# Kernel tuning notes

Hardware: AMD Instinct MI355X
Metric: run time of the kernel (lower is better)

## Reference

```python
import jax, jax.numpy as jnp
import numpy as np

N, E, D = 50000, 800000, 128
RESIDUAL_SCALE = 1.0
EPS = 1e-5  # torch LayerNorm default eps


def _mlp_ln(h, w1, b1, w2, b2, w3, b3, g, beta):
    # MeshGraphNets MLP: Linear -> SiLU -> Linear -> SiLU -> Linear -> LayerNorm
    h = jax.nn.silu(h @ w1 + b1)
    h = jax.nn.silu(h @ w2 + b2)
    h = h @ w3 + b3
    mu = h.mean(axis=-1, keepdims=True)
    var = ((h - mu) ** 2).mean(axis=-1, keepdims=True)
    return g * (h - mu) * jax.lax.rsqrt(var + EPS) + beta


def setup_inputs() -> dict:
    key = jax.random.key(0)
    ks = jax.random.split(key, 16)

    def lin(k, fan_in, fan_out):
        bound = 1.0 / np.sqrt(fan_in)
        kw, kb = jax.random.split(k)
        w = jax.random.uniform(kw, (fan_in, fan_out), jnp.float32, -bound, bound)
        b = jax.random.uniform(kb, (fan_out,), jnp.float32, -bound, bound)
        return w, b

    x = jax.random.normal(ks[0], (N, D), jnp.float32)
    edge_attr = jax.random.normal(ks[1], (E, D), jnp.float32)
    edge_index = jax.random.randint(ks[2], (2, E), 0, N, jnp.int32)

    ew1, eb1 = lin(ks[3], 3 * D, D)
    ew2, eb2 = lin(ks[4], D, D)
    ew3, eb3 = lin(ks[5], D, D)
    e_gamma = jnp.ones((D,), jnp.float32)
    e_beta = jnp.zeros((D,), jnp.float32)

    nw1, nb1 = lin(ks[6], 2 * D, D)
    nw2, nb2 = lin(ks[7], D, D)
    nw3, nb3 = lin(ks[8], D, D)
    n_gamma = jnp.ones((D,), jnp.float32)
    n_beta = jnp.zeros((D,), jnp.float32)

    return dict(x=x, edge_attr=edge_attr, edge_index=edge_index,
                ew1=ew1, eb1=eb1, ew2=ew2, eb2=eb2, ew3=ew3, eb3=eb3,
                e_gamma=e_gamma, e_beta=e_beta,
                nw1=nw1, nb1=nb1, nw2=nw2, nb2=nb2, nw3=nw3, nb3=nb3,
                n_gamma=n_gamma, n_beta=n_beta)


def reference(x, edge_attr, edge_index,
              ew1, eb1, ew2, eb2, ew3, eb3, e_gamma, e_beta,
              nw1, nb1, nw2, nb2, nw3, nb3, n_gamma, n_beta):
    senders, receivers = edge_index[0], edge_index[1]

    # EdgeBlock: gather endpoint node features, concat with edge_attr, MLP
    edge_in = jnp.concatenate([x[senders], x[receivers], edge_attr], axis=-1)  # [E, 3D]
    edge_mlp_out = _mlp_ln(edge_in, ew1, eb1, ew2, eb2, ew3, eb3, e_gamma, e_beta)  # [E, D]

    # NodeBlock: scatter-sum edge messages to receiver nodes, concat with x, MLP
    agg = jax.ops.segment_sum(edge_mlp_out, receivers, num_segments=N)  # [N, D]
    node_in = jnp.concatenate([x, agg], axis=-1)  # [N, 2D]
    node_mlp_out = _mlp_ln(node_in, nw1, nb1, nw2, nb2, nw3, nb3, n_gamma, n_beta)

    # Residual updates
    x_new = x + RESIDUAL_SCALE * node_mlp_out

    # PairNorm (use_pairnorm=True)
    x_centered = x_new - x_new.mean(axis=0, keepdims=True)
    rms = jnp.linalg.norm(x_centered) / jnp.sqrt(jnp.float32(x_new.shape[0])) + 1e-8
    x_new = x_centered / rms

    edge_attr_new = edge_attr + RESIDUAL_SCALE * edge_mlp_out
    return x_new, edge_attr_new
```

## Files before the change

### kernel.cpp

```cpp
#include <hip/hip_runtime.h>
#include <hip/hip_bf16.h>

#define NN 50000
#define NE 800000
#define ROWB 272

typedef unsigned short u16;
typedef unsigned int u32;
typedef __attribute__((ext_vector_type(4))) float f32x4;
typedef __attribute__((ext_vector_type(8))) short short8;


__device__ __forceinline__ u16 f2b(float f){ __hip_bfloat16 h = __float2bfloat16(f); u16 u; __builtin_memcpy(&u, &h, 2); return u; }
__device__ __forceinline__ float b2f(u16 u){ __hip_bfloat16 h; __builtin_memcpy(&h, &u, 2); return __bfloat162float(h); }
__device__ __forceinline__ float siluf(float v){
  const float e = __expf(-v);
  return v * __builtin_amdgcn_rcpf(1.f + e);
}

__device__ __forceinline__ uint4 cvt8(const float* __restrict__ s){
  const float4 a = *(const float4*)s;
  const float4 b = *(const float4*)(s + 4);
  union { u16 h[8]; uint4 q; } u;
  u.h[0]=f2b(a.x); u.h[1]=f2b(a.y); u.h[2]=f2b(a.z); u.h[3]=f2b(a.w);
  u.h[4]=f2b(b.x); u.h[5]=f2b(b.y); u.h[6]=f2b(b.z); u.h[7]=f2b(b.w);
  return u.q;
}

template<int K>
__device__ __forceinline__ void gemm128(f32x4 acc[4][2], const u16* __restrict__ sA,
                                        const u16* __restrict__ wB, int wm, int wn, int lane){
  const int l15 = lane & 15, l4 = lane >> 4;
  const u16* w0 = wB + (size_t)(wn*32 + l15)*K + l4*8;
  const u16* w1 = w0 + (size_t)16*K;
  #pragma unroll
  for (int ks = 0; ks < 4; ++ks){
    const short8 b0 = *(const short8*)(w0 + ks*32);
    const short8 b1 = *(const short8*)(w1 + ks*32);
    const int kb = ks*64 + l4*16;
    short8 a[4];
    #pragma unroll
    for (int fr = 0; fr < 4; ++fr)
      a[fr] = *(const short8*)((const char*)sA + (wm*64 + fr*16 + l15)*ROWB + kb);
    #pragma unroll
    for (int fr = 0; fr < 4; ++fr){
      acc[fr][0] = __builtin_amdgcn_mfma_f32_16x16x32_bf16(a[fr], b0, acc[fr][0], 0, 0, 0);
      acc[fr][1] = __builtin_amdgcn_mfma_f32_16x16x32_bf16(a[fr], b1, acc[fr][1], 0, 0, 0);
    }
  }
}

template<int K>
__device__ __forceinline__ void gemm64(f32x4 acc[2][4], const u16* __restrict__ sA,
                                       const u16* __restrict__ wB, int wm, int wn, int lane){
  const int l15 = lane & 15, l4 = lane >> 4;
  const u16* w0 = wB + (size_t)(wn*64 + l15)*K + l4*8;
  #pragma unroll
  for (int ks = 0; ks < 4; ++ks){
    short8 b[4];
    #pragma unroll
    for (int fc = 0; fc < 4; ++fc)
      b[fc] = *(const short8*)(w0 + (size_t)fc*16*K + ks*32);
    const int kb = ks*64 + l4*16;
    short8 a[2];
    #pragma unroll
    for (int fr = 0; fr < 2; ++fr)
      a[fr] = *(const short8*)((const char*)sA + (wm*32 + fr*16 + l15)*ROWB + kb);
    #pragma unroll
    for (int fr = 0; fr < 2; ++fr)
      #pragma unroll
      for (int fc = 0; fc < 4; ++fc)
        acc[fr][fc] = __builtin_amdgcn_mfma_f32_16x16x32_bf16(a[fr], b[fc], acc[fr][fc], 0, 0, 0);
  }
}

__device__ __forceinline__ void epilogue(const f32x4 acc[4][2], const float* __restrict__ bias,
                                         u16* __restrict__ dst, int wm, int wn, int lane, bool doSilu){
  const int l15 = lane & 15, l4 = lane >> 4;
  #pragma unroll
  for (int fc = 0; fc < 2; ++fc){
    const int col = wn*32 + fc*16 + l15;
    const float bv = bias[col];
    #pragma unroll
    for (int fr = 0; fr < 4; ++fr){
      const int rbase = wm*64 + fr*16 + l4*4;
      #pragma unroll
      for (int j = 0; j < 4; ++j){
        float v = acc[fr][fc][j] + bv;
        if (doSilu) v = siluf(v);
        *(u16*)((char*)dst + (rbase + j)*ROWB + col*2) = f2b(v);
      }
    }
  }
}

__device__ __forceinline__ void epilogue64(const f32x4 acc[2][4], const float* __restrict__ bias,
                                           u16* __restrict__ dst, int wm, int wn, int lane, bool doSilu){
  const int l15 = lane & 15, l4 = lane >> 4;
  #pragma unroll
  for (int fc = 0; fc < 4; ++fc){
    const int col = wn*64 + fc*16 + l15;
    const float bv = bias[col];
    #pragma unroll
    for (int fr = 0; fr < 2; ++fr){
      const int rbase = wm*32 + fr*16 + l4*4;
      #pragma unroll
      for (int j = 0; j < 4; ++j){
        float v = acc[fr][fc][j] + bv;
        if (doSilu) v = siluf(v);
        *(u16*)((char*)dst + (rbase + j)*ROWB + col*2) = f2b(v);
      }
    }
  }
}

__global__ __launch_bounds__(256) void prep_kernel(const float* __restrict__ w1, const float* __restrict__ w2,
                                                   const float* __restrict__ w3, const float* __restrict__ m1,
                                                   const float* __restrict__ m2, const float* __restrict__ m3,
                                                   u16* __restrict__ wt,
                                                   const float* __restrict__ x, u16* __restrict__ xB,
                                                   const int* __restrict__ eidx, int* __restrict__ cnt){
  const int i = blockIdx.x * 256 + threadIdx.x;
  if (i < 147456){
    const float* src; int K, base, off;
    if      (i < 49152)  { src = w1; K = 384; base = 0;      off = i; }
    else if (i < 65536)  { src = w2; K = 128; base = 49152;  off = i - 49152; }
    else if (i < 81920)  { src = w3; K = 128; base = 65536;  off = i - 65536; }
    else if (i < 114688) { src = m1; K = 256; base = 81920;  off = i - 81920; }
    else if (i < 131072) { src = m2; K = 128; base = 114688; off = i - 114688; }
    else                 { src = m3; K = 128; base = 131072; off = i - 131072; }
    const int k = off >> 7, n = off & 127;
    wt[base + n*K + k] = f2b(src[off]);
  }
  if (xB){
    const size_t o = (size_t)i * 8;
    *(uint4*)(xB + o) = cvt8(x + o);
  }
  atomicAdd(&cnt[eidx[NE + i]], 1);
}

__global__ __launch_bounds__(1024) void scan_kernel(const int* __restrict__ cnt, int* __restrict__ off,
                                                    int* __restrict__ cursor){
  __shared__ int s[1024];
  const int t = threadIdx.x;
  const int CH = 49;
  int sum = 0;
  for (int i = 0; i < CH; ++i){
    const int idx = t*CH + i;
    if (idx < NN) sum += cnt[idx];
  }
  s[t] = sum;
  __syncthreads();
  for (int d = 1; d < 1024; d <<= 1){
    int v = (t >= d) ? s[t - d] : 0;
    __syncthreads();
    s[t] += v;
    __syncthreads();
  }
  int run = s[t] - sum;
  for (int i = 0; i < CH; ++i){
    const int idx = t*CH + i;
    if (idx < NN){
      off[idx] = run;
      cursor[idx] = run;
      run += cnt[idx];
      if (idx == NN - 1) off[NN] = run;
    }
  }
}

__global__ __launch_bounds__(256) void scatter_kernel(const int* __restrict__ eidx, int* __restrict__ cursor,
                                                      int* __restrict__ perm, int* __restrict__ slot){
  const int i = blockIdx.x * 256 + threadIdx.x;
  if (i < NE){
    const int pos = atomicAdd(&cursor[eidx[NE + i]], 1);
    perm[pos] = i;
    slot[i] = pos;
  }
}

__global__ __launch_bounds__(256, 4) void pre_kernel(const float* __restrict__ x, const u16* __restrict__ xB,
                                                     const u16* __restrict__ wt, u16* __restrict__ Pab){
  __shared__ u16 sX[64*136];
  const int t = threadIdx.x;
  const int nBase = blockIdx.x * 64;
  const int lane = t & 63, wid = t >> 6;
  const int wm = wid >> 1, wn = wid & 1;
  const int chunk = t & 15, r0 = t >> 4;

  #pragma unroll
  for (int p = 0; p < 4; ++p){
    const int row = r0 + p*16;
    const int node = nBase + row;
    uint4 v = {0u, 0u, 0u, 0u};
    if (node < NN){
      if (xB) v = *(const uint4*)(xB + (size_t)node*128 + chunk*8);
      else    v = cvt8(x + (size_t)node*128 + chunk*8);
    }
    *(uint4*)((char*)sX + row*ROWB + chunk*16) = v;
  }
  __syncthreads();

  const f32x4 z4 = {0.f, 0.f, 0.f, 0.f};
  const int l15 = lane & 15, l4 = lane >> 4;
  #pragma unroll
  for (int half = 0; half < 2; ++half){
    f32x4 acc[2][4];
    #pragma unroll
    for (int fr = 0; fr < 2; ++fr)
      #pragma unroll
      for (int fc = 0; fc < 4; ++fc) acc[fr][fc] = z4;
    gemm64<384>(acc, sX, wt + half*128, wm, wn, lane);
    #pragma unroll
    for (int fc = 0; fc < 4; ++fc){
      const int col = wn*64 + fc*16 + l15;
      #pragma unroll
      for (int fr = 0; fr < 2; ++fr){
        const int rbase = wm*32 + fr*16 + l4*4;
        #pragma unroll
        for (int j = 0; j < 4; ++j){
          const int node = nBase + rbase + j;
          if (node < NN) Pab[(size_t)node*256 + half*128 + col] = f2b(acc[fr][fc][j]);
        }
      }
    }
  }
}

__global__ __launch_bounds__(512, 4) void edge_kernel(
    const float* __restrict__ ea, const int* __restrict__ eidx,
    const u16* __restrict__ wt, const u16* __restrict__ Pab,
    const float* __restrict__ b1, const float* __restrict__ b2,
    const float* __restrict__ b3, const float* __restrict__ gma, const float* __restrict__ bta,
    const int* __restrict__ slot, float* __restrict__ outE, u16* __restrict__ oBuf)
{
  __shared__ u16 sA[128*136];
  __shared__ float sMeta[640];
  __shared__ int sIdx[256];
  __shared__ int sSlot[128];
  const int t = threadIdx.x;
  const size_t eBase = (size_t)blockIdx.x * 128;

  if (t < 128){
    sIdx[t]       = eidx[eBase + t];
    sIdx[t + 128] = eidx[(size_t)NE + eBase + t];
    sSlot[t]      = slot[eBase + t];
    sMeta[t]       = b1[t];
    sMeta[t + 128] = b2[t];
    sMeta[t + 256] = b3[t];
    sMeta[t + 384] = gma[t];
    sMeta[t + 512] = bta[t];
  }
  __syncthreads();

  const int lane = t & 63, wid = t >> 6;
  const int wm = wid >> 2, wn = wid & 3;
  const int chunk = t & 15, r0 = t >> 4;
  const int l15 = lane & 15, l4 = lane >> 4;

  uint4 eaQ[4];
  #pragma unroll
  for (int p = 0; p < 4; ++p){
    const int row = r0 + p*32;
    uint4 v = cvt8(ea + ((eBase + row)*128 + chunk*8));
    eaQ[p] = v;
    *(uint4*)((char*)sA + row*ROWB + chunk*16) = v;
  }

  f32x4 acc[4][2];
  #pragma unroll
  for (int fr = 0; fr < 4; ++fr){
    #pragma unroll
    for (int j = 0; j < 4; ++j){
      const int row = wm*64 + fr*16 + l4*4 + j;
      const u16* pa = Pab + (size_t)sIdx[row]*256;
      const u16* pb = Pab + (size_t)sIdx[row + 128]*256 + 128;
      #pragma unroll
      for (int fc = 0; fc < 2; ++fc){
        const int col = wn*32 + fc*16 + l15;
        acc[fr][fc][j] = b2f(pa[col]) + b2f(pb[col]);
      }
    }
  }
  __syncthreads();

  gemm128<384>(acc, sA, wt + 256, wm, wn, lane);
  __syncthreads();
  epilogue(acc, sMeta + 0, sA, wm, wn, lane, true);
  __syncthreads();
  const f32x4 z4 = {0.f, 0.f, 0.f, 0.f};
  #pragma unroll
  for (int fr = 0; fr < 4; ++fr){ acc[fr][0] = z4; acc[fr][1] = z4; }
  gemm128<128>(acc, sA, wt + 49152, wm, wn, lane);
  __syncthreads();
  epilogue(acc, sMeta + 128, sA, wm, wn, lane, true);
  __syncthreads();
  #pragma unroll
  for (int fr = 0; fr < 4; ++fr){ acc[fr][0] = z4; acc[fr][1] = z4; }
  gemm128<128>(acc, sA, wt + 65536, wm, wn, lane);
  __syncthreads();
  epilogue(acc, sMeta + 256, sA, wm, wn, lane, false);
  __syncthreads();

  {
    #pragma unroll
    for (int p = 0; p < 4; ++p){
      const int row = r0 + p*32;
      uint4 q = *(const uint4*)((const char*)sA + row*ROWB + chunk*16);
      const u16* pu = (const u16*)&q;
      float h[8];
      #pragma unroll
      for (int j = 0; j < 8; ++j) h[j] = b2f(pu[j]);
      float s = 0.f;
      #pragma unroll
      for (int j = 0; j < 8; ++j) s += h[j];
      s += __shfl_xor(s, 1); s += __shfl_xor(s, 2); s += __shfl_xor(s, 4); s += __shfl_xor(s, 8);
      const float mu = s * (1.f/128.f);
      float ss = 0.f;
      #pragma unroll
      for (int j = 0; j < 8; ++j){ const float d = h[j] - mu; ss += d*d; }
      ss += __shfl_xor(ss, 1); ss += __shfl_xor(ss, 2); ss += __shfl_xor(ss, 4); ss += __shfl_xor(ss, 8);
      const float rs = rsqrtf(fmaxf(ss*(1.f/128.f), 0.f) + 1e-5f);
      const size_t e = eBase + row;
      const u16* ep = (const u16*)&eaQ[p];
      alignas(16) float orow[8];
      alignas(16) u16 obf[8];
      #pragma unroll
      for (int j = 0; j < 8; ++j){
        const int col = chunk*8 + j;
        const float o = sMeta[384 + col]*(h[j] - mu)*rs + sMeta[512 + col];
        orow[j] = b2f(ep[j]) + o;
        obf[j] = f2b(o);
      }
      float* dst = outE + e*128 + chunk*8;
      *(float4*)dst       = ((const float4*)orow)[0];
      *(float4*)(dst + 4) = ((const float4*)orow)[1];
      if (oBuf) *(uint4*)(oBuf + (size_t)sSlot[row]*128 + chunk*8) = *(const uint4*)obf;
    }
  }
}

__global__ __launch_bounds__(256) void agg_f_kernel(const float* __restrict__ outE, const float* __restrict__ ea,
                                                    const int* __restrict__ off, const int* __restrict__ perm,
                                                    float* __restrict__ agg){
  const int node = blockIdx.x * 4 + (threadIdx.x >> 6);
  const int lane = threadIdx.x & 63;
  if (node >= NN) return;
  const int s = off[node], e = off[node + 1];
  float a0 = 0.f, a1 = 0.f;
  for (int i = s; i < e; ++i){
    const size_t r = (size_t)perm[i] * 128;
    a0 += outE[r + lane]      - ea[r + lane];
    a1 += outE[r + 64 + lane] - ea[r + 64 + lane];
  }
  agg[(size_t)node*128 + lane]      = a0;
  agg[(size_t)node*128 + 64 + lane] = a1;
}

__global__ __launch_bounds__(256, 4) void node_kernel(
    const float* __restrict__ x, const float* __restrict__ aggF,
    const u16* __restrict__ oBuf, const int* __restrict__ off,
    const u16* __restrict__ wt,
    const float* __restrict__ b1, const float* __restrict__ b2, const float* __restrict__ b3,
    const float* __restrict__ gma, const float* __restrict__ bta,
    float* __restrict__ outX, float* __restrict__ stats)
{
  __shared__ u16 sA[64*136];
  __shared__ float sMeta[640];
  __shared__ float sCol[128];
  __shared__ float sSq;
  const int t = threadIdx.x;
  const int nBase = blockIdx.x * 64;

  if (t < 128){
    sMeta[t]       = b1[t];
    sMeta[t + 128] = b2[t];
    sMeta[t + 256] = b3[t];
    sMeta[t + 384] = gma[t];
    sMeta[t + 512] = bta[t];
    sCol[t] = 0.f;
  }
  if (t == 0) sSq = 0.f;
  __syncthreads();

  const int lane = t & 63, wid = t >> 6;
  const int wm = wid >> 1, wn = wid & 1;
  const int chunk = t & 15, r0 = t >> 4;

  const f32x4 z4 = {0.f, 0.f, 0.f, 0.f};
  f32x4 acc[2][4];
  #pragma unroll
  for (int fr = 0; fr < 2; ++fr)
    #pragma unroll
    for (int fc = 0; fc < 4; ++fc) acc[fr][fc] = z4;

  for (int kc = 0; kc < 2; ++kc){
    #pragma unroll
    for (int p = 0; p < 4; ++p){
      const int row = r0 + p*16;
      const int node = nBase + row;
      uint4 v = {0u, 0u, 0u, 0u};
      if (node < NN){
        if (kc == 0){
          v = cvt8(x + (size_t)node*128 + chunk*8);
        } else if (oBuf){
          float a[8] = {0.f,0.f,0.f,0.f,0.f,0.f,0.f,0.f};
          const int s0 = off[node], e0 = off[node + 1];
          for (int i = s0; i < e0; ++i){
            uint4 q = *(const uint4*)(oBuf + (size_t)i*128 + chunk*8);
            const u16* pu = (const u16*)&q;
            #pragma unroll
            for (int j = 0; j < 8; ++j) a[j] += b2f(pu[j]);
          }
          union { u16 h[8]; uint4 q; } u;
          #pragma unroll
          for (int j = 0; j < 8; ++j) u.h[j] = f2b(a[j]);
          v = u.q;
        } else {
          v = cvt8(aggF + (size_t)node*128 + chunk*8);
        }
      }
      *(uint4*)((char*)sA + row*ROWB + chunk*16) = v;
    }
    __syncthreads();
    gemm64<256>(acc, sA, wt + 81920 + kc*128, wm, wn, lane);
    __syncthreads();
  }
  epilogue64(acc, sMeta + 0, sA, wm, wn, lane, true);
  __syncthreads();
  #pragma unroll
  for (int fr = 0; fr < 2; ++fr)
    #pragma unroll
    for (int fc = 0; fc < 4; ++fc) acc[fr][fc] = z4;
  gemm64<128>(acc, sA, wt + 114688, wm, wn, lane);
  __syncthreads();
  epilogue64(acc, sMeta + 128, sA, wm, wn, lane, true);
  __syncthreads();
  #pragma unroll
  for (int fr = 0; fr < 2; ++fr)
    #pragma unroll
    for (int fc = 0; fc < 4; ++fc) acc[fr][fc] = z4;
  gemm64<128>(acc, sA, wt + 131072, wm, wn, lane);
  __syncthreads();
  epilogue64(acc, sMeta + 256, sA, wm, wn, lane, false);
  __syncthreads();

  {
    float lssq = 0.f;
    #pragma unroll
    for (int p = 0; p < 4; ++p){
      const int row = r0 + p*16;
      const int node = nBase + row;
      uint4 q = *(const uint4*)((const char*)sA + row*ROWB + chunk*16);
      const u16* pu = (const u16*)&q;
      float h[8];
      #pragma unroll
      for (int j = 0; j < 8; ++j) h[j] = b2f(pu[j]);
      float s = 0.f;
      #pragma unroll
      for (int j = 0; j < 8; ++j) s += h[j];
      s += __shfl_xor(s, 1); s += __shfl_xor(s, 2); s += __shfl_xor(s, 4); s += __shfl_xor(s, 8);
      const float mu = s * (1.f/128.f);
      float ss = 0.f;
      #pragma unroll
      for (int j = 0; j < 8; ++j){ const float d = h[j] - mu; ss += d*d; }
      ss += __shfl_xor(ss, 1); ss += __shfl_xor(ss, 2); ss += __shfl_xor(ss, 4); ss += __shfl_xor(ss, 8);
      const float rs = rsqrtf(fmaxf(ss*(1.f/128.f), 0.f) + 1e-5f);
      if (node < NN){
        const float* xRow = x + (size_t)node*128 + chunk*8;
        const float4 xa = *(const float4*)xRow;
        const float4 xb = *(const float4*)(xRow + 4);
        float xr[8] = {xa.x, xa.y, xa.z, xa.w, xb.x, xb.y, xb.z, xb.w};
        alignas(16) float orow[8];
        #pragma unroll
        for (int j = 0; j < 8; ++j){
          const int col = chunk*8 + j;
          const float o = sMeta[384 + col]*(h[j] - mu)*rs + sMeta[512 + col];
          const float res = xr[j] + o;
          orow[j] = res;
          atomicAdd(&sCol[col], res);
          lssq += res*res;
        }
        float* dst = outX + (size_t)node*128 + chunk*8;
        *(float4*)dst       = ((const float4*)orow)[0];
        *(float4*)(dst + 4) = ((const float4*)orow)[1];
      }
    }
    #pragma unroll
    for (int m = 1; m < 64; m <<= 1) lssq += __shfl_xor(lssq, m);
    if (lane == 0) atomicAdd(&sSq, lssq);
  }
  __syncthreads();
  if (t < 128) atomicAdd(&stats[t], sCol[t]);
  if (t == 0)  atomicAdd(&stats[128], sSq);
}

__global__ __launch_bounds__(256) void pairnorm_kernel(float* __restrict__ xOut, const float* __restrict__ stats){
  __shared__ float sMean[128];
  __shared__ float sP2[2];
  __shared__ float sInv;
  const int t = threadIdx.x;
  float m2 = 0.f;
  if (t < 128){
    const float mean = stats[t] * (1.f / (float)NN);
    sMean[t] = mean;
    m2 = mean * mean;
  }
  #pragma unroll
  for (int m = 1; m < 64; m <<= 1) m2 += __shfl_xor(m2, m);
  if ((t & 63) == 0 && t < 128) sP2[t >> 6] = m2;
  __syncthreads();
  if (t == 0){
    float ssc = stats[128] - (float)NN * (sP2[0] + sP2[1]);
    ssc = fmaxf(ssc, 0.f);
    const float rms = sqrtf(ssc * (1.f / (float)NN)) + 1e-8f;
    sInv = 1.f / rms;
  }
  __syncthreads();
  const size_t base = ((size_t)blockIdx.x * 256 + t) * 4;
  const int col = (int)(base & 127);
  float4 q = *(float4*)(xOut + base);
  const float inv = sInv;
  q.x = (q.x - sMean[col])     * inv;
  q.y = (q.y - sMean[col + 1]) * inv;
  q.z = (q.z - sMean[col + 2]) * inv;
  q.w = (q.w - sMean[col + 3]) * inv;
  *(float4*)(xOut + base) = q;
}

extern "C" void kernel_launch(void* const* d_in, const int* in_sizes, int n_in,
                              void* d_out, int out_size, void* d_ws, size_t ws_size,
                              hipStream_t stream){
  (void)in_sizes; (void)n_in; (void)out_size;
  const float* x    = (const float*)d_in[0];
  const float* ea   = (const float*)d_in[1];
  const int*   eidx = (const int*)d_in[2];
  const float* ew1  = (const float*)d_in[3];
  const float* eb1  = (const float*)d_in[4];
  const float* ew2  = (const float*)d_in[5];
  const float* eb2  = (const float*)d_in[6];
  const float* ew3  = (const float*)d_in[7];
  const float* eb3  = (const float*)d_in[8];
  const float* eg   = (const float*)d_in[9];
  const float* ebt  = (const float*)d_in[10];
  const float* nw1  = (const float*)d_in[11];
  const float* nb1  = (const float*)d_in[12];
  const float* nw2  = (const float*)d_in[13];
  const float* nb2  = (const float*)d_in[14];
  const float* nw3  = (const float*)d_in[15];
  const float* nb3  = (const float*)d_in[16];
  const float* ng   = (const float*)d_in[17];
  const float* nbt  = (const float*)d_in[18];

  u16*   wt     = (u16*)d_ws;
  float* stats  = (float*)((char*)d_ws + 294912);
  int*   cnt    = (int*)((char*)d_ws + 297216);
  int*   off    = (int*)((char*)d_ws + 497408);
  int*   cursor = (int*)((char*)d_ws + 697600);
  int*   perm   = (int*)((char*)d_ws + 897792);
  int*   slot   = (int*)((char*)d_ws + 4097792);
  const bool useO = ws_size >= (7297792ull + (size_t)NE * 128 * 2);
  const bool useX = ws_size >= (7297792ull + (size_t)NE * 128 * 2 + (size_t)NN * 128 * 2);
  u16*   oBuf   = useO ? (u16*)((char*)d_ws + 7297792) : (u16*)nullptr;
  u16*   xB     = useX ? (u16*)((char*)d_ws + 7297792 + (size_t)NE * 128 * 2) : (u16*)nullptr;
  float* outX   = (float*)d_out;
  u16*   Pab    = (u16*)d_out;
  float* outE   = outX + (size_t)NN * 128;

  hipMemsetAsync(stats, 0, 2048, stream);
  hipMemsetAsync(cnt, 0, NN * sizeof(int), stream);
  prep_kernel<<<3125, 256, 0, stream>>>(ew1, ew2, ew3, nw1, nw2, nw3, wt, x, xB, eidx, cnt);
  scan_kernel<<<1, 1024, 0, stream>>>(cnt, off, cursor);
  scatter_kernel<<<3125, 256, 0, stream>>>(eidx, cursor, perm, slot);
  pre_kernel<<<782, 256, 0, stream>>>(x, xB, wt, Pab);
  edge_kernel<<<6250, 512, 0, stream>>>(ea, eidx, wt, Pab, eb1, eb2, eb3, eg, ebt, slot, outE, oBuf);
  if (!useO) agg_f_kernel<<<12500, 256, 0, stream>>>(outE, ea, off, perm, outX);
  node_kernel<<<782, 256, 0, stream>>>(x, outX, oBuf, off, wt, nb1, nb2, nb3, ng, nbt, outX, stats);
  pairnorm_kernel<<<6250, 256, 0, stream>>>(outX, stats);
}
```

Baseline: 723.2 us.

## Fuse scan into precompute kernel and assign CSR slots inside edge kernel

Merges the single-block prefix scan into the node precompute kernel as an extra block, and drops the separate scatter pass on the bf16 output path by claiming each edge's CSR slot with an atomic on the cursor inside the edge kernel. The two memsets are combined into one. This removes kernel launches and a full pass over edge indices. In exchange the scan now runs on 256 threads instead of 1024. Slot order within a segment becomes nondeterministic, and the edge kernel's atomics contend on hot receivers.

```diff
diff --git a/kernel.cpp b/kernel.cpp
--- a/kernel.cpp
+++ b/kernel.cpp
@@ -139,51 +139,51 @@
   atomicAdd(&cnt[eidx[NE + i]], 1);
 }
 
-__global__ __launch_bounds__(1024) void scan_kernel(const int* __restrict__ cnt, int* __restrict__ off,
-                                                    int* __restrict__ cursor){
-  __shared__ int s[1024];
-  const int t = threadIdx.x;
-  const int CH = 49;
-  int sum = 0;
-  for (int i = 0; i < CH; ++i){
-    const int idx = t*CH + i;
-    if (idx < NN) sum += cnt[idx];
-  }
-  s[t] = sum;
-  __syncthreads();
-  for (int d = 1; d < 1024; d <<= 1){
-    int v = (t >= d) ? s[t - d] : 0;
-    __syncthreads();
-    s[t] += v;
-    __syncthreads();
-  }
-  int run = s[t] - sum;
-  for (int i = 0; i < CH; ++i){
-    const int idx = t*CH + i;
-    if (idx < NN){
-      off[idx] = run;
-      cursor[idx] = run;
-      run += cnt[idx];
-      if (idx == NN - 1) off[NN] = run;
-    }
-  }
-}
-
 __global__ __launch_bounds__(256) void scatter_kernel(const int* __restrict__ eidx, int* __restrict__ cursor,
-                                                      int* __restrict__ perm, int* __restrict__ slot){
+                                                      int* __restrict__ perm){
   const int i = blockIdx.x * 256 + threadIdx.x;
   if (i < NE){
     const int pos = atomicAdd(&cursor[eidx[NE + i]], 1);
     perm[pos] = i;
-    slot[i] = pos;
-  }
-}
-
-__global__ __launch_bounds__(256, 4) void pre_kernel(const float* __restrict__ x, const u16* __restrict__ xB,
-                                                     const u16* __restrict__ wt, u16* __restrict__ Pab){
+  }
+}
+
+__global__ __launch_bounds__(256, 4) void scanpre_kernel(const int* __restrict__ cnt, int* __restrict__ off,
+                                                         int* __restrict__ cursor,
+                                                         const float* __restrict__ x, const u16* __restrict__ xB,
+                                                         const u16* __restrict__ wt, u16* __restrict__ Pab){
+  const int t = threadIdx.x;
+  if (blockIdx.x == 0){
+    __shared__ int s[256];
+    const int CH = 196;
+    int sum = 0;
+    for (int i = 0; i < CH; ++i){
+      const int idx = t*CH + i;
+      if (idx < NN) sum += cnt[idx];
+    }
+    s[t] = sum;
+    __syncthreads();
+    for (int d = 1; d < 256; d <<= 1){
+      int v = (t >= d) ? s[t - d] : 0;
+      __syncthreads();
+      s[t] += v;
+      __syncthreads();
+    }
+    int run = s[t] - sum;
+    for (int i = 0; i < CH; ++i){
+      const int idx = t*CH + i;
+      if (idx < NN){
+        off[idx] = run;
+        cursor[idx] = run;
+        run += cnt[idx];
+        if (idx == NN - 1) off[NN] = run;
+      }
+    }
+    return;
+  }
+
   __shared__ u16 sX[64*136];
-  const int t = threadIdx.x;
-  const int nBase = blockIdx.x * 64;
+  const int nBase = (blockIdx.x - 1) * 64;
   const int lane = t & 63, wid = t >> 6;
   const int wm = wid >> 1, wn = wid & 1;
   const int chunk = t & 15, r0 = t >> 4;
@@ -232,7 +232,7 @@
     const u16* __restrict__ wt, const u16* __restrict__ Pab,
     const float* __restrict__ b1, const float* __restrict__ b2,
     const float* __restrict__ b3, const float* __restrict__ gma, const float* __restrict__ bta,
-    const int* __restrict__ slot, float* __restrict__ outE, u16* __restrict__ oBuf)
+    int* __restrict__ cursor, float* __restrict__ outE, u16* __restrict__ oBuf)
 {
   __shared__ u16 sA[128*136];
   __shared__ float sMeta[640];
@@ -242,9 +242,10 @@
   const size_t eBase = (size_t)blockIdx.x * 128;
 
   if (t < 128){
-    sIdx[t]       = eidx[eBase + t];
-    sIdx[t + 128] = eidx[(size_t)NE + eBase + t];
-    sSlot[t]      = slot[eBase + t];
+    sIdx[t] = eidx[eBase + t];
+    const int r = eidx[(size_t)NE + eBase + t];
+    sIdx[t + 128] = r;
+    if (oBuf) sSlot[t] = atomicAdd(&cursor[r], 1);
     sMeta[t]       = b1[t];
     sMeta[t + 128] = b2[t];
     sMeta[t + 256] = b3[t];
@@ -558,7 +559,6 @@
   int*   off    = (int*)((char*)d_ws + 497408);
   int*   cursor = (int*)((char*)d_ws + 697600);
   int*   perm   = (int*)((char*)d_ws + 897792);
-  int*   slot   = (int*)((char*)d_ws + 4097792);
   const bool useO = ws_size >= (7297792ull + (size_t)NE * 128 * 2);
   const bool useX = ws_size >= (7297792ull + (size_t)NE * 128 * 2 + (size_t)NN * 128 * 2);
   u16*   oBuf   = useO ? (u16*)((char*)d_ws + 7297792) : (u16*)nullptr;
@@ -567,13 +567,11 @@
   u16*   Pab    = (u16*)d_out;
   float* outE   = outX + (size_t)NN * 128;
 
-  hipMemsetAsync(stats, 0, 2048, stream);
-  hipMemsetAsync(cnt, 0, NN * sizeof(int), stream);
+  hipMemsetAsync((char*)d_ws + 294912, 0, 202496, stream);
   prep_kernel<<<3125, 256, 0, stream>>>(ew1, ew2, ew3, nw1, nw2, nw3, wt, x, xB, eidx, cnt);
-  scan_kernel<<<1, 1024, 0, stream>>>(cnt, off, cursor);
-  scatter_kernel<<<3125, 256, 0, stream>>>(eidx, cursor, perm, slot);
-  pre_kernel<<<782, 256, 0, stream>>>(x, xB, wt, Pab);
-  edge_kernel<<<6250, 512, 0, stream>>>(ea, eidx, wt, Pab, eb1, eb2, eb3, eg, ebt, slot, outE, oBuf);
+  scanpre_kernel<<<783, 256, 0, stream>>>(cnt, off, cursor, x, xB, wt, Pab);
+  if (!useO) scatter_kernel<<<3125, 256, 0, stream>>>(eidx, cursor, perm);
+  edge_kernel<<<6250, 512, 0, stream>>>(ea, eidx, wt, Pab, eb1, eb2, eb3, eg, ebt, cursor, outE, oBuf);
   if (!useO) agg_f_kernel<<<12500, 256, 0, stream>>>(outE, ea, off, perm, outX);
   node_kernel<<<782, 256, 0, stream>>>(x, outX, oBuf, off, wt, nb1, nb2, nb3, ng, nbt, outX, stats);
   pairnorm_kernel<<<6250, 256, 0, stream>>>(outX, stats);
```

After: 685.4 us. 5.2% less time.
